# Kernel optimization log

Measured on AMD Instinct MI355X. Metric: run time of the kernel, lower is better.

Reference implementation:

```python
import jax, jax.numpy as jnp
import numpy as np


def setup_inputs() -> dict:
    key = jax.random.key(0)
    k1, k2, k3, k4 = jax.random.split(key, 4)
    B, S, D_IN, D_OUT = 4, 2048, 1024, 1024
    x = jax.random.normal(k1, (B, S, D_IN), dtype=jnp.float32)
    # torch Linear weights: shape [d_out, d_in], scaled like kaiming-uniform-ish init
    scale = 1.0 / np.sqrt(D_IN)
    Wq = jax.random.normal(k2, (D_OUT, D_IN), dtype=jnp.float32) * scale
    Wk = jax.random.normal(k3, (D_OUT, D_IN), dtype=jnp.float32) * scale
    Wv = jax.random.normal(k4, (D_OUT, D_IN), dtype=jnp.float32) * scale
    return {"x": x, "Wq": Wq, "Wk": Wk, "Wv": Wv}


def reference(x, Wq, Wk, Wv):
    # x: [B, S, d_in]; W*: [d_out, d_in] (torch Linear convention y = x @ W.T)
    q = jnp.einsum("bsd,od->bso", x, Wq)
    k = jnp.einsum("bsd,od->bso", x, Wk)
    v = jnp.einsum("bsd,od->bso", x, Wv)
    d_out = k.shape[-1]
    scores = jnp.einsum("bqo,bko->bqk", q, k)  # [B, S, S]
    S = scores.shape[-1]
    causal = jnp.tril(jnp.ones((S, S), dtype=bool))  # True where allowed
    scores = jnp.where(causal, scores, -jnp.inf)
    weights = jax.nn.softmax(scores / jnp.sqrt(jnp.float32(d_out)), axis=-1)
    return jnp.einsum("bqk,bko->bqo", weights, v)
```

## Files before the change

kernel.cpp:

```cpp
#include <hip/hip_runtime.h>
#include <hip/hip_bf16.h>
#include <stdint.h>

typedef short bf16x8 __attribute__((ext_vector_type(8)));
typedef float f32x4 __attribute__((ext_vector_type(4)));

__device__ __forceinline__ float b2f(unsigned short u) {
    union { unsigned int i; float f; } c; c.i = ((unsigned int)u) << 16; return c.f;
}
__device__ __forceinline__ unsigned short f2b(float f) {
    union { float f; unsigned int i; } c; c.f = f;
    unsigned int u = c.i;
    u += 0x7fffu + ((u >> 16) & 1u);
    return (unsigned short)(u >> 16);
}

__device__ __forceinline__ void gload_lds16(const void* g, void* l) {
    __builtin_amdgcn_global_load_lds(
        (const __attribute__((address_space(1))) void*)g,
        (__attribute__((address_space(3))) void*)l, 16, 0, 0);
}

__global__ __launch_bounds__(256) void f32_to_bf16(const float* __restrict__ in,
                                                   unsigned short* __restrict__ out,
                                                   long n4) {
    long i = (long)blockIdx.x * blockDim.x + threadIdx.x;
    long stride = (long)gridDim.x * blockDim.x;
    for (; i < n4; i += stride) {
        float4 v = ((const float4*)in)[i];
        ushort4 o;
        o.x = f2b(v.x); o.y = f2b(v.y); o.z = f2b(v.z); o.w = f2b(v.w);
        ((ushort4*)out)[i] = o;
    }
}

__global__ __launch_bounds__(256) void transpose_bf16(const unsigned short* __restrict__ in,
                                                      unsigned short* __restrict__ out,
                                                      int S, int D) {
    __shared__ unsigned short tile[64][65];
    int d0 = blockIdx.x * 64, s0 = blockIdx.y * 64;
    long base = (long)blockIdx.z * S * D;
    int c = threadIdx.x & 63, rg = threadIdx.x >> 6;
    #pragma unroll
    for (int i = 0; i < 16; i++) {
        int r = rg * 16 + i;
        tile[r][c] = in[base + (long)(s0 + r) * D + d0 + c];
    }
    __syncthreads();
    #pragma unroll
    for (int i = 0; i < 16; i++) {
        int r = rg * 16 + i;
        out[base + (long)(d0 + r) * S + s0 + c] = tile[c][r];
    }
}

__global__ __launch_bounds__(256) void softmax_causal(unsigned short* __restrict__ Sb, int S) {
    int rowid = blockIdx.x;
    int b = rowid / S, q = rowid - b * S;
    unsigned short* p = Sb + ((long)b * S + q) * S;
    int t = threadIdx.x, lane = t & 63, wid = t >> 6;
    __shared__ float rmax[4], rsum[4];

    float v[8];
    float mx = -3e38f;
    #pragma unroll
    for (int i = 0; i < 8; i++) {
        int k = i * 256 + t;
        float x = (k <= q) ? b2f(p[k]) : -3e38f;
        v[i] = x; mx = fmaxf(mx, x);
    }
    #pragma unroll
    for (int o = 1; o < 64; o <<= 1) mx = fmaxf(mx, __shfl_xor(mx, o));
    if (lane == 0) rmax[wid] = mx;
    __syncthreads();
    mx = fmaxf(fmaxf(rmax[0], rmax[1]), fmaxf(rmax[2], rmax[3]));

    float s = 0.f;
    #pragma unroll
    for (int i = 0; i < 8; i++) {
        int k = i * 256 + t;
        float e = (k <= q) ? __expf(v[i] - mx) : 0.f;
        v[i] = e; s += e;
    }
    #pragma unroll
    for (int o = 1; o < 64; o <<= 1) s += __shfl_xor(s, o);
    if (lane == 0) rsum[wid] = s;
    __syncthreads();
    s = rsum[0] + rsum[1] + rsum[2] + rsum[3];
    float inv = 1.f / s;
    #pragma unroll
    for (int i = 0; i < 8; i++) {
        p[i * 256 + t] = f2b(v[i] * inv);
    }
}

#define BM 128
#define BN 128
#define BK 64

template <int MODE>
__global__ __launch_bounds__(256)
void gemm_bt(const unsigned short* __restrict__ A, const unsigned short* __restrict__ B,
             void* __restrict__ C0, void* __restrict__ C1, void* __restrict__ C2,
             int M, int N, int K,
             long sA, long sB, long sC, int lda, int ldb, int ldc) {
    int mb = blockIdx.y, nb = blockIdx.x, bz = blockIdx.z;
    if (MODE == 1 && nb > mb) return;

    __shared__ unsigned short As[BM * BK];
    __shared__ unsigned short Bs[BN * BK];

    const unsigned short* Ab = A + (long)bz * sA;
    const unsigned short* Bb = B + (long)bz * sB;

    const int t = threadIdx.x;
    const int lane = t & 63;
    const int wid = t >> 6;
    const int wr = wid >> 1, wc = wid & 1;
    const int m0 = mb * BM, n0 = nb * BN;

    int Keff = K;
    if (MODE == 2) Keff = min(K, m0 + BM);

    f32x4 acc[4][4];
    #pragma unroll
    for (int i = 0; i < 4; i++)
        #pragma unroll
        for (int j = 0; j < 4; j++) acc[i][j] = (f32x4){0.f, 0.f, 0.f, 0.f};

    int rowS[4], csrc[4];
    #pragma unroll
    for (int i = 0; i < 4; i++) {
        int u = i * 256 + t;
        rowS[i] = u >> 3;
        csrc[i] = (u & 7) ^ (rowS[i] & 7);
    }

    for (int k0 = 0; k0 < Keff; k0 += BK) {
        __syncthreads();
        #pragma unroll
        for (int i = 0; i < 4; i++) {
            const unsigned short* gp = Ab + (long)(m0 + rowS[i]) * lda + k0 + csrc[i] * 8;
            gload_lds16(gp, (void*)&As[(i * 256 + wid * 64) * 8]);
        }
        #pragma unroll
        for (int i = 0; i < 4; i++) {
            const unsigned short* gp = Bb + (long)(n0 + rowS[i]) * ldb + k0 + csrc[i] * 8;
            gload_lds16(gp, (void*)&Bs[(i * 256 + wid * 64) * 8]);
        }
        asm volatile("s_waitcnt vmcnt(0)" ::: "memory");
        __syncthreads();

        #pragma unroll
        for (int s = 0; s < 2; s++) {
            bf16x8 af[4], bfr[4];
            int kc = s * 4 + (lane >> 4);
            #pragma unroll
            for (int m = 0; m < 4; m++) {
                int r = wr * 64 + m * 16 + (lane & 15);
                int c = kc ^ (r & 7);
                af[m] = *(const bf16x8*)&As[r * BK + c * 8];
            }
            #pragma unroll
            for (int n = 0; n < 4; n++) {
                int r = wc * 64 + n * 16 + (lane & 15);
                int c = kc ^ (r & 7);
                bfr[n] = *(const bf16x8*)&Bs[r * BK + c * 8];
            }
            #pragma unroll
            for (int m = 0; m < 4; m++)
                #pragma unroll
                for (int n = 0; n < 4; n++)
                    acc[m][n] = __builtin_amdgcn_mfma_f32_16x16x32_bf16(af[m], bfr[n], acc[m][n], 0, 0, 0);
        }
    }

    const int r0 = (lane >> 4) * 4;
    const int cf = lane & 15;
    if (MODE == 0) {
        int buf = n0 >> 10;
        unsigned short* Cb = (unsigned short*)(buf == 0 ? C0 : (buf == 1 ? C1 : C2));
        float scale = (buf == 0) ? 0.03125f : 1.0f;
        #pragma unroll
        for (int m = 0; m < 4; m++)
            #pragma unroll
            for (int n = 0; n < 4; n++)
                #pragma unroll
                for (int r = 0; r < 4; r++) {
                    long grow = m0 + wr * 64 + m * 16 + r0 + r;
                    int gcol = (n0 & 1023) + wc * 64 + n * 16 + cf;
                    Cb[grow * 1024 + gcol] = f2b(acc[m][n][r] * scale);
                }
    } else if (MODE == 1) {
        unsigned short* Cb = (unsigned short*)C0 + (long)bz * sC;
        #pragma unroll
        for (int m = 0; m < 4; m++)
            #pragma unroll
            for (int n = 0; n < 4; n++)
                #pragma unroll
                for (int r = 0; r < 4; r++) {
                    long grow = m0 + wr * 64 + m * 16 + r0 + r;
                    int gcol = n0 + wc * 64 + n * 16 + cf;
                    Cb[grow * ldc + gcol] = f2b(acc[m][n][r]);
                }
    } else {
        float* Cb = (float*)C0 + (long)bz * sC;
        #pragma unroll
        for (int m = 0; m < 4; m++)
            #pragma unroll
            for (int n = 0; n < 4; n++)
                #pragma unroll
                for (int r = 0; r < 4; r++) {
                    long grow = m0 + wr * 64 + m * 16 + r0 + r;
                    int gcol = n0 + wc * 64 + n * 16 + cf;
                    Cb[grow * ldc + gcol] = acc[m][n][r];
                }
    }
}

extern "C" void kernel_launch(void* const* d_in, const int* in_sizes, int n_in,
                              void* d_out, int out_size, void* d_ws, size_t ws_size,
                              hipStream_t stream) {
    const float* x  = (const float*)d_in[0];
    const float* Wq = (const float*)d_in[1];
    const float* Wk = (const float*)d_in[2];
    const float* Wv = (const float*)d_in[3];

    char* ws = (char*)d_ws;
    unsigned short* xb = (unsigned short*)(ws);
    unsigned short* wb = (unsigned short*)(ws + 16777216);
    unsigned short* Qb = (unsigned short*)(ws + 23068672);
    unsigned short* Kb = (unsigned short*)(ws + 39845888);
    unsigned short* Vb = (unsigned short*)(ws + 56623104);
    unsigned short* Vt = (unsigned short*)(ws + 73400320);
    unsigned short* Sb = (unsigned short*)(ws + 90177536);

    f32_to_bf16<<<dim3(2048), dim3(256), 0, stream>>>(x, xb, 8388608L / 4);
    f32_to_bf16<<<dim3(256), dim3(256), 0, stream>>>(Wq, wb,           1048576L / 4);
    f32_to_bf16<<<dim3(256), dim3(256), 0, stream>>>(Wk, wb + 1048576, 1048576L / 4);
    f32_to_bf16<<<dim3(256), dim3(256), 0, stream>>>(Wv, wb + 2097152, 1048576L / 4);

    gemm_bt<0><<<dim3(24, 64, 1), 256, 0, stream>>>(
        xb, wb, Qb, Kb, Vb, 8192, 3072, 1024, 0L, 0L, 0L, 1024, 1024, 1024);

    transpose_bf16<<<dim3(16, 32, 4), 256, 0, stream>>>(Vb, Vt, 2048, 1024);

    gemm_bt<1><<<dim3(16, 16, 4), 256, 0, stream>>>(
        Qb, Kb, Sb, nullptr, nullptr, 2048, 2048, 1024,
        2048L * 1024, 2048L * 1024, 2048L * 2048, 1024, 1024, 2048);

    softmax_causal<<<dim3(8192), dim3(256), 0, stream>>>(Sb, 2048);

    gemm_bt<2><<<dim3(8, 16, 4), 256, 0, stream>>>(
        Sb, Vt, d_out, nullptr, nullptr, 2048, 1024, 2048,
        2048L * 2048, 1024L * 2048, 2048L * 1024, 2048, 2048, 1024);
}
```

Baseline: 194.0 us.

## Merge conversions, compact causal grid, vectorize transpose and trim softmax work

Merges the four fp32-to-bf16 conversion launches into one kernel. Replaces the square score-GEMM grid, where upper-triangle blocks exited early, with a compact triangular grid of 136 blocks per batch. Launches the PV GEMM with the heaviest rows first. Vectorizes the transpose's global loads and stores and makes softmax read and write only the causal prefix with 16-byte accesses, skipping the fully masked tail. This cuts launch overhead, idle blocks and masked memory traffic. The trade-offs are a per-block sqrt to decode the triangle index and the reliance that softmax-skipped columns are never read later, since PV limits K to the block's causal extent.

```diff
diff --git a/kernel.cpp b/kernel.cpp
--- a/kernel.cpp
+++ b/kernel.cpp
@@ -21,16 +21,33 @@
         (__attribute__((address_space(3))) void*)l, 16, 0, 0);
 }
 
-__global__ __launch_bounds__(256) void f32_to_bf16(const float* __restrict__ in,
-                                                   unsigned short* __restrict__ out,
-                                                   long n4) {
+__global__ __launch_bounds__(256) void convert_all(const float* __restrict__ x,
+                                                   const float* __restrict__ Wq,
+                                                   const float* __restrict__ Wk,
+                                                   const float* __restrict__ Wv,
+                                                   unsigned short* __restrict__ xb,
+                                                   unsigned short* __restrict__ wb) {
+    const long X4 = 2097152, W4 = 262144, TOT = X4 + 3 * W4;
     long i = (long)blockIdx.x * blockDim.x + threadIdx.x;
     long stride = (long)gridDim.x * blockDim.x;
-    for (; i < n4; i += stride) {
-        float4 v = ((const float4*)in)[i];
+    for (; i < TOT; i += stride) {
+        const float4* src;
+        ushort4* dst;
+        if (i < X4) {
+            src = (const float4*)x + i;
+            dst = (ushort4*)xb + i;
+        } else {
+            long j = i - X4;
+            int w = (int)(j >> 18);
+            long off = j & (W4 - 1);
+            const float* s = (w == 0) ? Wq : (w == 1) ? Wk : Wv;
+            src = (const float4*)s + off;
+            dst = (ushort4*)wb + (long)w * W4 + off;
+        }
+        float4 v = *src;
         ushort4 o;
         o.x = f2b(v.x); o.y = f2b(v.y); o.z = f2b(v.z); o.w = f2b(v.w);
-        ((ushort4*)out)[i] = o;
+        *dst = o;
     }
 }
 
@@ -40,17 +57,24 @@
     __shared__ unsigned short tile[64][65];
     int d0 = blockIdx.x * 64, s0 = blockIdx.y * 64;
     long base = (long)blockIdx.z * S * D;
-    int c = threadIdx.x & 63, rg = threadIdx.x >> 6;
-    #pragma unroll
-    for (int i = 0; i < 16; i++) {
-        int r = rg * 16 + i;
-        tile[r][c] = in[base + (long)(s0 + r) * D + d0 + c];
+    int t = threadIdx.x;
+    #pragma unroll
+    for (int it = 0; it < 4; it++) {
+        int u = it * 256 + t;
+        int r = u >> 4, c4 = (u & 15) * 4;
+        ushort4 v = *(const ushort4*)&in[base + (long)(s0 + r) * D + d0 + c4];
+        tile[r][c4 + 0] = v.x; tile[r][c4 + 1] = v.y;
+        tile[r][c4 + 2] = v.z; tile[r][c4 + 3] = v.w;
     }
     __syncthreads();
     #pragma unroll
-    for (int i = 0; i < 16; i++) {
-        int r = rg * 16 + i;
-        out[base + (long)(d0 + r) * S + s0 + c] = tile[c][r];
+    for (int it = 0; it < 4; it++) {
+        int u = it * 256 + t;
+        int rr = u >> 4, c4 = (u & 15) * 4;
+        ushort4 o;
+        o.x = tile[c4 + 0][rr]; o.y = tile[c4 + 1][rr];
+        o.z = tile[c4 + 2][rr]; o.w = tile[c4 + 3][rr];
+        *(ushort4*)&out[base + (long)(d0 + rr) * S + s0 + c4] = o;
     }
 }
 
@@ -59,15 +83,23 @@
     int b = rowid / S, q = rowid - b * S;
     unsigned short* p = Sb + ((long)b * S + q) * S;
     int t = threadIdx.x, lane = t & 63, wid = t >> 6;
+    int wl = (q & ~127) + 128;
+    int nv = wl >> 3;
     __shared__ float rmax[4], rsum[4];
 
     float v[8];
     float mx = -3e38f;
-    #pragma unroll
-    for (int i = 0; i < 8; i++) {
-        int k = i * 256 + t;
-        float x = (k <= q) ? b2f(p[k]) : -3e38f;
-        v[i] = x; mx = fmaxf(mx, x);
+    if (t < nv) {
+        bf16x8 in8 = *(const bf16x8*)&p[t * 8];
+        #pragma unroll
+        for (int j = 0; j < 8; j++) {
+            int k = t * 8 + j;
+            float x = (k <= q) ? b2f((unsigned short)in8[j]) : -3e38f;
+            v[j] = x; mx = fmaxf(mx, x);
+        }
+    } else {
+        #pragma unroll
+        for (int j = 0; j < 8; j++) v[j] = -3e38f;
     }
     #pragma unroll
     for (int o = 1; o < 64; o <<= 1) mx = fmaxf(mx, __shfl_xor(mx, o));
@@ -77,10 +109,10 @@
 
     float s = 0.f;
     #pragma unroll
-    for (int i = 0; i < 8; i++) {
-        int k = i * 256 + t;
-        float e = (k <= q) ? __expf(v[i] - mx) : 0.f;
-        v[i] = e; s += e;
+    for (int j = 0; j < 8; j++) {
+        int k = t * 8 + j;
+        float e = (t < nv && k <= q) ? __expf(v[j] - mx) : 0.f;
+        v[j] = e; s += e;
     }
     #pragma unroll
     for (int o = 1; o < 64; o <<= 1) s += __shfl_xor(s, o);
@@ -88,9 +120,12 @@
     __syncthreads();
     s = rsum[0] + rsum[1] + rsum[2] + rsum[3];
     float inv = 1.f / s;
-    #pragma unroll
-    for (int i = 0; i < 8; i++) {
-        p[i * 256 + t] = f2b(v[i] * inv);
+
+    if (t < nv) {
+        bf16x8 o8;
+        #pragma unroll
+        for (int j = 0; j < 8; j++) o8[j] = (short)f2b(v[j] * inv);
+        *(bf16x8*)&p[t * 8] = o8;
     }
 }
 
@@ -99,17 +134,12 @@
 #define BK 64
 
 template <int MODE>
-__global__ __launch_bounds__(256)
-void gemm_bt(const unsigned short* __restrict__ A, const unsigned short* __restrict__ B,
-             void* __restrict__ C0, void* __restrict__ C1, void* __restrict__ C2,
-             int M, int N, int K,
-             long sA, long sB, long sC, int lda, int ldb, int ldc) {
-    int mb = blockIdx.y, nb = blockIdx.x, bz = blockIdx.z;
-    if (MODE == 1 && nb > mb) return;
-
-    __shared__ unsigned short As[BM * BK];
-    __shared__ unsigned short Bs[BN * BK];
-
+__device__ __forceinline__
+void gemm_body(unsigned short* As, unsigned short* Bs,
+               const unsigned short* __restrict__ A, const unsigned short* __restrict__ B,
+               void* __restrict__ C0, void* __restrict__ C1, void* __restrict__ C2,
+               int mb, int nb, int bz, int K,
+               long sA, long sB, long sC, int lda, int ldb, int ldc) {
     const unsigned short* Ab = A + (long)bz * sA;
     const unsigned short* Bb = B + (long)bz * sB;
 
@@ -218,6 +248,39 @@
     }
 }
 
+__global__ __launch_bounds__(256)
+void gemm_qkv(const unsigned short* __restrict__ A, const unsigned short* __restrict__ B,
+              void* C0, void* C1, void* C2, int K, int lda, int ldb) {
+    __shared__ unsigned short As[BM * BK];
+    __shared__ unsigned short Bs[BN * BK];
+    gemm_body<0>(As, Bs, A, B, C0, C1, C2, blockIdx.y, blockIdx.x, 0, K,
+                 0L, 0L, 0L, lda, ldb, 0);
+}
+
+__global__ __launch_bounds__(256)
+void gemm_scores(const unsigned short* __restrict__ A, const unsigned short* __restrict__ B,
+                 void* C0, int K, long sA, long sB, long sC, int lda, int ldb, int ldc) {
+    __shared__ unsigned short As[BM * BK];
+    __shared__ unsigned short Bs[BN * BK];
+    int l = blockIdx.x;
+    int mb = (int)((sqrtf(8.f * l + 1.f) - 1.f) * 0.5f);
+    while ((mb + 1) * (mb + 2) / 2 <= l) mb++;
+    while (mb * (mb + 1) / 2 > l) mb--;
+    int nb = l - mb * (mb + 1) / 2;
+    gemm_body<1>(As, Bs, A, B, C0, nullptr, nullptr, mb, nb, blockIdx.z, K,
+                 sA, sB, sC, lda, ldb, ldc);
+}
+
+__global__ __launch_bounds__(256)
+void gemm_pv(const unsigned short* __restrict__ A, const unsigned short* __restrict__ B,
+             void* C0, int K, long sA, long sB, long sC, int lda, int ldb, int ldc) {
+    __shared__ unsigned short As[BM * BK];
+    __shared__ unsigned short Bs[BN * BK];
+    int mb = gridDim.y - 1 - blockIdx.y;
+    gemm_body<2>(As, Bs, A, B, C0, nullptr, nullptr, mb, blockIdx.x, blockIdx.z, K,
+                 sA, sB, sC, lda, ldb, ldc);
+}
+
 extern "C" void kernel_launch(void* const* d_in, const int* in_sizes, int n_in,
                               void* d_out, int out_size, void* d_ws, size_t ws_size,
                               hipStream_t stream) {
@@ -235,23 +298,19 @@
     unsigned short* Vt = (unsigned short*)(ws + 73400320);
     unsigned short* Sb = (unsigned short*)(ws + 90177536);
 
-    f32_to_bf16<<<dim3(2048), dim3(256), 0, stream>>>(x, xb, 8388608L / 4);
-    f32_to_bf16<<<dim3(256), dim3(256), 0, stream>>>(Wq, wb,           1048576L / 4);
-    f32_to_bf16<<<dim3(256), dim3(256), 0, stream>>>(Wk, wb + 1048576, 1048576L / 4);
-    f32_to_bf16<<<dim3(256), dim3(256), 0, stream>>>(Wv, wb + 2097152, 1048576L / 4);
-
-    gemm_bt<0><<<dim3(24, 64, 1), 256, 0, stream>>>(
-        xb, wb, Qb, Kb, Vb, 8192, 3072, 1024, 0L, 0L, 0L, 1024, 1024, 1024);
+    convert_all<<<dim3(2048), dim3(256), 0, stream>>>(x, Wq, Wk, Wv, xb, wb);
+
+    gemm_qkv<<<dim3(24, 64, 1), 256, 0, stream>>>(xb, wb, Qb, Kb, Vb, 1024, 1024, 1024);
 
     transpose_bf16<<<dim3(16, 32, 4), 256, 0, stream>>>(Vb, Vt, 2048, 1024);
 
-    gemm_bt<1><<<dim3(16, 16, 4), 256, 0, stream>>>(
-        Qb, Kb, Sb, nullptr, nullptr, 2048, 2048, 1024,
+    gemm_scores<<<dim3(136, 1, 4), 256, 0, stream>>>(
+        Qb, Kb, Sb, 1024,
         2048L * 1024, 2048L * 1024, 2048L * 2048, 1024, 1024, 2048);
 
     softmax_causal<<<dim3(8192), dim3(256), 0, stream>>>(Sb, 2048);
 
-    gemm_bt<2><<<dim3(8, 16, 4), 256, 0, stream>>>(
-        Sb, Vt, d_out, nullptr, nullptr, 2048, 1024, 2048,
+    gemm_pv<<<dim3(8, 16, 4), 256, 0, stream>>>(
+        Sb, Vt, d_out, 2048,
         2048L * 2048, 1024L * 2048, 2048L * 1024, 2048, 2048, 1024);
 }
```

Measured after the change: 192.4 us. No clear change (-0.8%).
